# Kernel optimization log

Measured on AMD Instinct MI355X. Metric: run time of the kernel, lower is better.

Reference implementation:

```python
import jax, jax.numpy as jnp
import numpy as np

B, S, V = 16, 256, 32000
E, H, L, FFN, NC = 256, 8, 2, 1024, 4
DK = E // H
NQ = E  # n_qubits == hidden_dim == embed_dim (required by the module's shape constraints)
EPS = 1e-5


def qproj(x, theta):
    # Analytic simulation of: RX(x_k) encode + trainable RX(theta_k) + CNOT ladder + MeasureAll(PauliZ).
    # RX gates on the same wire compose; CNOT ladder maps Z_j -> Z_0...Z_j in Heisenberg picture, so
    # <Z_j> = prod_{k<=j} cos(x_k + theta_k)  (product state expectation).
    return jnp.cumprod(jnp.cos(x + theta), axis=-1)


def layernorm(x, g, b):
    m = x.mean(-1, keepdims=True)
    v = x.var(-1, keepdims=True)
    return (x - m) * jax.lax.rsqrt(v + EPS) * g + b


def sinusoidal_pe(seq, d):
    pos = jnp.arange(seq, dtype=jnp.float32)[:, None]
    div = jnp.exp(jnp.arange(0, d, 2, dtype=jnp.float32) * (-np.log(10000.0) / d))
    pe = jnp.zeros((seq, d), jnp.float32)
    pe = pe.at[:, 0::2].set(jnp.sin(pos * div)).at[:, 1::2].set(jnp.cos(pos * div))
    return pe


def _forward(x, token_emb, lstm_W, lstm_b, lstm_theta, ln1_g, ln1_b, ln2_g, ln2_b,
             qkv_theta, combine_W, combine_b, ffn_theta, lin1_W, lin1_b, lin2_W, lin2_b,
             cls_W, cls_b):
    emb = token_emb[x]  # (B, S, E)

    # --- QLSTM: each gate = linear -> quantum circuit -> nonlinearity ---
    def step(carry, xt):
        hx, cx = carry
        comb = jnp.concatenate([xt, hx], axis=-1)                      # (B, 2E)
        z = jnp.einsum('bd,gdq->gbq', comb, lstm_W) + lstm_b[:, None]  # (4, B, NQ)
        q = jnp.cumprod(jnp.cos(z + lstm_theta[:, None, :]), axis=-1)
        f = jax.nn.sigmoid(q[0])
        i = jax.nn.sigmoid(q[1])
        g = jnp.tanh(q[2])
        o = jax.nn.sigmoid(q[3])
        cx = f * cx + i * g
        hx = o * jnp.tanh(cx)
        return (hx, cx), hx

    h0 = jnp.zeros((emb.shape[0], NQ), emb.dtype)
    _, hs = jax.lax.scan(step, (h0, h0), jnp.swapaxes(emb, 0, 1))
    h = jnp.swapaxes(hs, 0, 1)  # (B, S, NQ)

    h = h + sinusoidal_pe(h.shape[1], E)[None]

    # --- quantum transformer blocks ---
    def heads(t):
        return t.reshape(t.shape[0], t.shape[1], H, DK).transpose(0, 2, 1, 3)

    for l in range(L):
        q = qproj(h, qkv_theta[l, 0])
        k = qproj(h, qkv_theta[l, 1])
        v = qproj(h, qkv_theta[l, 2])
        qh, kh, vh = heads(q), heads(k), heads(v)
        scores = jnp.einsum('bhqd,bhkd->bhqk', qh, kh) / jnp.sqrt(jnp.float32(DK))
        attn = jax.nn.softmax(scores, axis=-1)
        out = jnp.einsum('bhqk,bhkd->bhqd', attn, vh).transpose(0, 2, 1, 3).reshape(h.shape)
        out = out @ combine_W[l] + combine_b[l]
        h = layernorm(h + out, ln1_g[l], ln1_b[l])
        ff = qproj(h, ffn_theta[l]) @ lin1_W[l] + lin1_b[l]
        ff = jax.nn.relu(ff) @ lin2_W[l] + lin2_b[l]
        h = layernorm(h + ff, ln2_g[l], ln2_b[l])

    pooled = h.mean(axis=1)  # (B, E)
    return pooled @ cls_W + cls_b  # (B, NC)


def setup_inputs() -> dict:
    key = jax.random.key(0)
    ks = jax.random.split(key, 10)
    s = 0.05
    return {
        'x': jax.random.randint(ks[0], (B, S), 0, V),
        'token_emb': jax.random.normal(ks[1], (V, E), jnp.float32) * s,
        'lstm_W': jax.random.normal(ks[2], (4, 2 * E, NQ), jnp.float32) * s,
        'lstm_b': jnp.zeros((4, NQ), jnp.float32),
        'lstm_theta': jax.random.normal(ks[3], (4, NQ), jnp.float32) * s,
        'ln1_g': jnp.ones((L, E), jnp.float32),
        'ln1_b': jnp.zeros((L, E), jnp.float32),
        'ln2_g': jnp.ones((L, E), jnp.float32),
        'ln2_b': jnp.zeros((L, E), jnp.float32),
        'qkv_theta': jax.random.normal(ks[4], (L, 3, E), jnp.float32) * s,
        'combine_W': jax.random.normal(ks[5], (L, E, E), jnp.float32) * s,
        'combine_b': jnp.zeros((L, E), jnp.float32),
        'ffn_theta': jax.random.normal(ks[6], (L, E), jnp.float32) * s,
        'lin1_W': jax.random.normal(ks[7], (L, E, FFN), jnp.float32) * s,
        'lin1_b': jnp.zeros((L, FFN), jnp.float32),
        'lin2_W': jax.random.normal(ks[8], (L, FFN, E), jnp.float32) * s,
        'lin2_b': jnp.zeros((L, E), jnp.float32),
        'cls_W': jax.random.normal(ks[9], (E, NC), jnp.float32) * s,
        'cls_b': jnp.zeros((NC,), jnp.float32),
    }


def reference(x, token_emb, lstm_W, lstm_b, lstm_theta, ln1_g, ln1_b, ln2_g, ln2_b,
              qkv_theta, combine_W, combine_b, ffn_theta, lin1_W, lin1_b, lin2_W, lin2_b,
              cls_W, cls_b):
    return _forward(x, token_emb, lstm_W, lstm_b, lstm_theta, ln1_g, ln1_b, ln2_g, ln2_b,
                    qkv_theta, combine_W, combine_b, ffn_theta, lin1_W, lin1_b, lin2_W, lin2_b,
                    cls_W, cls_b)
```

## Files before the change

kernel.cpp:

```cpp
#include <hip/hip_runtime.h>
#include <hip/hip_bf16.h>


typedef __attribute__((ext_vector_type(8))) short bf8v;
typedef __attribute__((ext_vector_type(4))) float f4v;
#define MFMA16 __builtin_amdgcn_mfma_f32_16x16x32_bf16

__device__ __forceinline__ unsigned short f2bf(float f) {
  unsigned u = __builtin_bit_cast(unsigned, f);
  u += 0x7fffu + ((u >> 16) & 1u);
  return (unsigned short)(u >> 16);
}
__device__ __forceinline__ float rcp_f(float x) { return __builtin_amdgcn_rcpf(x); }
__device__ __forceinline__ float sigm(float x) { return rcp_f(1.f + __expf(-x)); }
__device__ __forceinline__ float tanh_f(float x) { return 1.f - 2.f * rcp_f(__expf(2.f * x) + 1.f); }

#define DOT2BF(acc, a, b) \
  asm("v_dot2_f32_bf16 %0, %1, %2, %0" : "+v"(acc) : "v"(a), "v"(b))

__global__ void embed_kernel(const int* __restrict__ x, const float* __restrict__ tab,
                             unsigned short* __restrict__ eb) {
  int tok = blockIdx.x, tid = threadIdx.x;
  eb[tok * 256 + tid] = f2bf(tab[x[tok] * 256 + tid]);
}

__global__ void pack_bt(const float* __restrict__ W, int K, int N,
                        unsigned short* __restrict__ Th, long wz, long tz) {
  __shared__ float tile[64][65];
  W += (long)blockIdx.z * wz;
  Th += (long)blockIdx.z * tz;
  int n0 = blockIdx.x * 64, k0 = blockIdx.y * 64;
  int tid = threadIdx.x, tx = tid & 63, ty = tid >> 6;
  for (int r = ty; r < 64; r += 4) tile[r][tx] = W[(k0 + r) * N + n0 + tx];
  __syncthreads();
  for (int r = ty; r < 64; r += 4) {
    Th[(n0 + r) * K + k0 + tx] = f2bf(tile[tx][r]);
  }
}

__global__ void pack_wreg_kernel(const float* __restrict__ lstmW, unsigned* __restrict__ Wreg) {
  int o = blockIdx.x * 256 + threadIdx.x;
  int c = o & 3;
  int q = (o >> 2) & 255;
  int i4 = (o >> 10) & 15;
  int gs = o >> 14;
  int gi = gs >> 1, s = gs & 1;
  int i = i4 * 4 + c;
  int d = s * 128 + 2 * i;
  unsigned lo = f2bf(lstmW[(gi * 512 + 256 + d) * 256 + q]);
  unsigned hi = f2bf(lstmW[(gi * 512 + 256 + d + 1) * 256 + q]);
  Wreg[o] = lo | (hi << 16);
}

__global__ void pack_wl_kernel(const float* __restrict__ lstmW, unsigned* __restrict__ WLg) {
  int o = blockIdx.x * 256 + threadIdx.x;
  int c = o & 3;
  int q = (o >> 2) & 255;
  int p4 = o >> 10;
  int d = 2 * (p4 * 4 + c);
  unsigned lo = f2bf(lstmW[(3 * 512 + 256 + d) * 256 + q]);
  unsigned hi = f2bf(lstmW[(3 * 512 + 256 + d + 1) * 256 + q]);
  WLg[o] = lo | (hi << 16);
}

__global__ void __launch_bounds__(256) gemm_mfma(const unsigned short* __restrict__ A,
                                                 const unsigned short* __restrict__ B,
                                                 const float* __restrict__ bias,
                                                 float* __restrict__ Cf,
                                                 unsigned short* __restrict__ Cb,
                                                 int M, int N, int K, int mode) {
  __shared__ unsigned short As[128 * 40];
  __shared__ unsigned short Bs[128 * 40];

  const int tid = threadIdx.x;
  const int lane = tid & 63;
  const int wid = tid >> 6;
  const int wr = wid >> 1, wc = wid & 1;
  const int bm = blockIdx.y * 128, bn = blockIdx.x * 128;

  const int srow = tid >> 2;
  const int scol = (tid & 3) * 8;

  f4v acc[4][4] = {};

  for (int kt = 0; kt < K; kt += 32) {
#pragma unroll
    for (int p = 0; p < 2; ++p) {
      int r = srow + p * 64;
      *(uint4*)(&As[r * 40 + scol]) = *(const uint4*)(&A[(bm + r) * K + kt + scol]);
      *(uint4*)(&Bs[r * 40 + scol]) = *(const uint4*)(&B[(bn + r) * K + kt + scol]);
    }
    __syncthreads();

    bf8v a[4], b[4];
    const int kq = (lane >> 4) * 8;
#pragma unroll
    for (int f = 0; f < 4; ++f) {
      a[f] = *(const bf8v*)(&As[(wr * 64 + f * 16 + (lane & 15)) * 40 + kq]);
      b[f] = *(const bf8v*)(&Bs[(wc * 64 + f * 16 + (lane & 15)) * 40 + kq]);
    }
#pragma unroll
    for (int fm = 0; fm < 4; ++fm)
#pragma unroll
      for (int fn = 0; fn < 4; ++fn)
        acc[fm][fn] = MFMA16(a[fm], b[fn], acc[fm][fn], 0, 0, 0);
    __syncthreads();
  }

#pragma unroll
  for (int fm = 0; fm < 4; ++fm)
#pragma unroll
    for (int fn = 0; fn < 4; ++fn) {
      int c = bn + wc * 64 + fn * 16 + (lane & 15);
      int r0 = bm + wr * 64 + fm * 16 + ((lane >> 4) << 2);
      float bv = bias[c];
#pragma unroll
      for (int j = 0; j < 4; ++j) {
        float v = acc[fm][fn][j] + bv;
        if (mode == 1) {
          Cb[(r0 + j) * N + c] = f2bf(fmaxf(v, 0.f));
        } else {
          Cf[(r0 + j) * N + c] = v;
        }
      }
    }
}

__global__ void
__attribute__((amdgpu_flat_work_group_size(512, 512), amdgpu_waves_per_eu(2, 2)))
lstm_kernel(const unsigned* __restrict__ Wreg,
            const unsigned* __restrict__ WLg,
            const float* __restrict__ lstmTh,
            const float* __restrict__ xw,
            float* __restrict__ hb) {
  extern __shared__ char smem[];
  unsigned* WL = (unsigned*)smem;
  float* part = (float*)(smem + 131072);
  float* qv = part + 2048;
  float* wtot = qv + 1024;
  unsigned* hp = (unsigned*)(wtot + 16);

  const int t = threadIdx.x;
  const int b = blockIdx.x;
  const int q = t & 255;
  const int s = t >> 8;
  const int lane = t & 63;
  const int w = t >> 6;

  {
    const uint4* src = (const uint4*)WLg;
    uint4* dst = (uint4*)WL;
    for (int j = t; j < 8192; j += 512) dst[j] = src[j];
  }
  const uint4* Wreg4 = (const uint4*)Wreg;
  uint4 wreg[48];
#pragma unroll
  for (int j = 0; j < 48; ++j) {
    int gi = j >> 4, i4 = j & 15;
    wreg[j] = Wreg4[((gi * 2 + s) * 16 + i4) * 256 + q];
  }
#pragma unroll
  for (int j = 0; j < 48; ++j) {
    asm volatile("" : "+v"(wreg[j].x), "+v"(wreg[j].y), "+v"(wreg[j].z), "+v"(wreg[j].w));
  }
  const float thA = lstmTh[t];
  const float thB = lstmTh[512 + t];
  float cx = 0.f;
  if (t < 128) hp[t] = 0u;
  __syncthreads();

  const int xbase = (b << 8) * 1024;
  const uint4* WL4 = (const uint4*)WL;
  const uint4* hp4 = (const uint4*)hp;

  float xa = xw[xbase + t];
  float xb = xw[xbase + 512 + t];

  for (int st = 0; st < 256; ++st) {
    int nx = (st < 255) ? st + 1 : 255;
    float xa_n = xw[xbase + nx * 1024 + t];
    float xb_n = xw[xbase + nx * 1024 + 512 + t];

    float a0 = 0.f, a1 = 0.f, a2 = 0.f, a3 = 0.f;
#pragma unroll
    for (int i4 = 0; i4 < 16; ++i4) {
      uint4 hh = hp4[(s << 4) + i4];
      uint4 w3 = WL4[((s << 4) + i4) * 256 + q];
      uint4 w0 = wreg[i4];
      uint4 w1 = wreg[16 + i4];
      uint4 w2 = wreg[32 + i4];
      DOT2BF(a0, w0.x, hh.x); DOT2BF(a0, w0.y, hh.y);
      DOT2BF(a0, w0.z, hh.z); DOT2BF(a0, w0.w, hh.w);
      DOT2BF(a1, w1.x, hh.x); DOT2BF(a1, w1.y, hh.y);
      DOT2BF(a1, w1.z, hh.z); DOT2BF(a1, w1.w, hh.w);
      DOT2BF(a2, w2.x, hh.x); DOT2BF(a2, w2.y, hh.y);
      DOT2BF(a2, w2.z, hh.z); DOT2BF(a2, w2.w, hh.w);
      DOT2BF(a3, w3.x, hh.x); DOT2BF(a3, w3.y, hh.y);
      DOT2BF(a3, w3.z, hh.z); DOT2BF(a3, w3.w, hh.w);
    }
    part[(0 * 2 + s) * 256 + q] = a0;
    part[(1 * 2 + s) * 256 + q] = a1;
    part[(2 * 2 + s) * 256 + q] = a2;
    part[(3 * 2 + s) * 256 + q] = a3;
    __syncthreads();

    int gA = s, gB = s + 2;
    float zA = part[(gA * 2 + 0) * 256 + q] + part[(gA * 2 + 1) * 256 + q] + xa + thA;
    float zB = part[(gB * 2 + 0) * 256 + q] + part[(gB * 2 + 1) * 256 + q] + xb + thB;
    float vA = __cosf(zA);
    float vB = __cosf(zB);
#pragma unroll
    for (int off = 1; off < 64; off <<= 1) {
      float oA = __shfl_up(vA, off, 64);
      float oB = __shfl_up(vB, off, 64);
      if (lane >= off) { vA *= oA; vB *= oB; }
    }
    if (lane == 63) { wtot[w * 2] = vA; wtot[w * 2 + 1] = vB; }
    qv[s * 256 + q] = vA;
    qv[512 + s * 256 + q] = vB;
    __syncthreads();

    if (t < 256) {
      int j = q >> 6;
      float p0 = 1.f, p1 = 1.f, p2 = 1.f, p3 = 1.f;
      for (int k = 0; k < j; ++k) {
        p0 *= wtot[2 * k];
        p1 *= wtot[2 * (4 + k)];
        p2 *= wtot[2 * k + 1];
        p3 *= wtot[2 * (4 + k) + 1];
      }
      float fg = sigm(qv[t] * p0);
      float ig = sigm(qv[256 + t] * p1);
      float gg = tanh_f(qv[512 + t] * p2);
      float og = sigm(qv[768 + t] * p3);
      cx = fg * cx + ig * gg;
      float hv = og * tanh_f(cx);
      hb[((b << 8) + st) * 256 + t] = hv;
      float nb = __shfl_xor(hv, 1, 64);
      if ((t & 1) == 0) hp[t >> 1] = (unsigned)f2bf(hv) | ((unsigned)f2bf(nb) << 16);
    }
    __syncthreads();
    xa = xa_n;
    xb = xb_n;
  }
}

__global__ void pe_add_kernel(float* __restrict__ h) {
  int tok = blockIdx.x, tid = threadIdx.x;
  int s = tok & 255;
  int j = tid >> 1;
  float div = __expf((float)j * -0.07195578415622253f);
  float ang = (float)s * div;
  float pe = (tid & 1) ? __cosf(ang) : __sinf(ang);
  h[tok * 256 + tid] += pe;
}

__global__ void qproj3_kernel(const float* __restrict__ hin, const float* __restrict__ thetas,
                              float* __restrict__ outbase) {
  __shared__ float wtot[4];
  int tok = blockIdx.x, y = blockIdx.y;
  int tid = threadIdx.x, lane = tid & 63, wid = tid >> 6;
  const float* theta = thetas + y * 256;
  float* out = outbase + (long)y * 1048576;
  float v = __cosf(hin[tok * 256 + tid] + theta[tid]);
#pragma unroll
  for (int off = 1; off < 64; off <<= 1) {
    float o = __shfl_up(v, off, 64);
    if (lane >= off) v *= o;
  }
  if (lane == 63) wtot[wid] = v;
  __syncthreads();
  float pre = 1.f;
  for (int w = 0; w < wid; ++w) pre *= wtot[w];
  out[tok * 256 + tid] = v * pre;
}

__global__ void qproj_bf_kernel(const float* __restrict__ hin, const float* __restrict__ theta,
                                unsigned short* __restrict__ outb) {
  __shared__ float wtot[4];
  int tok = blockIdx.x, tid = threadIdx.x, lane = tid & 63, wid = tid >> 6;
  float v = __cosf(hin[tok * 256 + tid] + theta[tid]);
#pragma unroll
  for (int off = 1; off < 64; off <<= 1) {
    float o = __shfl_up(v, off, 64);
    if (lane >= off) v *= o;
  }
  if (lane == 63) wtot[wid] = v;
  __syncthreads();
  float pre = 1.f;
  for (int w = 0; w < wid; ++w) pre *= wtot[w];
  outb[tok * 256 + tid] = f2bf(v * pre);
}

__global__ void __launch_bounds__(256, 1) attn_kernel(const float* __restrict__ qb,
                                                      const float* __restrict__ kb,
                                                      const float* __restrict__ vb,
                                                      unsigned short* __restrict__ outb) {
  extern __shared__ float sm[];
  float* Qs = sm;
  float* Ks = Qs + 256 * 36;
  float* Vs = Ks + 256 * 36;
  float* ps = Vs + 32 * 260;
  int hd = blockIdx.x, b = blockIdx.y;
  int tid = threadIdx.x, lane = tid & 63, wid = tid >> 6;
  const float scale = 0.17677669529663687f;

  for (int i = tid; i < 256 * 32; i += 256) {
    int r = i >> 5, d = i & 31;
    int src = (b * 256 + r) * 256 + hd * 32 + d;
    Qs[r * 36 + d] = qb[src];
    Ks[r * 36 + d] = kb[src];
    Vs[d * 260 + r] = vb[src];
  }
  __syncthreads();

  float* pw = ps + wid * 256;
  for (int r = wid; r < 256; r += 4) {
    float4 qreg[8];
    const float4* qrow = (const float4*)(Qs + r * 36);
#pragma unroll
    for (int i = 0; i < 8; ++i) qreg[i] = qrow[i];
    float s[4];
#pragma unroll
    for (int j = 0; j < 4; ++j) {
      int k = lane + 64 * j;
      const float4* kr = (const float4*)(Ks + k * 36);
      float a = 0.f;
#pragma unroll
      for (int i = 0; i < 8; ++i) {
        float4 kv = kr[i];
        a += qreg[i].x * kv.x + qreg[i].y * kv.y + qreg[i].z * kv.z + qreg[i].w * kv.w;
      }
      s[j] = a * scale;
    }
    float m = fmaxf(fmaxf(s[0], s[1]), fmaxf(s[2], s[3]));
#pragma unroll
    for (int off = 32; off; off >>= 1) m = fmaxf(m, __shfl_xor(m, off, 64));
    float p[4], sum = 0.f;
#pragma unroll
    for (int j = 0; j < 4; ++j) { p[j] = __expf(s[j] - m); sum += p[j]; }
#pragma unroll
    for (int off = 32; off; off >>= 1) sum += __shfl_xor(sum, off, 64);
    float inv = rcp_f(sum);
#pragma unroll
    for (int j = 0; j < 4; ++j) pw[lane + 64 * j] = p[j] * inv;
    int d = lane & 31, half = lane >> 5;
    const float4* pv = (const float4*)(pw + half * 128);
    const float4* v4 = (const float4*)(Vs + d * 260 + half * 128);
    float a = 0.f;
#pragma unroll
    for (int i = 0; i < 32; ++i) {
      float4 pp = pv[i];
      float4 vv = v4[i];
      a += pp.x * vv.x + pp.y * vv.y + pp.z * vv.z + pp.w * vv.w;
    }
    a += __shfl_down(a, 32, 64);
    if (lane < 32) outb[(b * 256 + r) * 256 + hd * 32 + d] = f2bf(a);
  }
}

__global__ void ln_kernel(float* __restrict__ hio, const float* __restrict__ delta,
                          const float* __restrict__ gamma, const float* __restrict__ beta) {
  __shared__ float red[16];
  int tok = blockIdx.x, tid = threadIdx.x, lane = tid & 63, wid = tid >> 6;
  float v = hio[tok * 256 + tid] + delta[tok * 256 + tid];
  float s1 = v, s2 = v * v;
#pragma unroll
  for (int off = 32; off; off >>= 1) {
    s1 += __shfl_xor(s1, off, 64);
    s2 += __shfl_xor(s2, off, 64);
  }
  if (lane == 0) { red[wid] = s1; red[wid + 8] = s2; }
  __syncthreads();
  float t1 = red[0] + red[1] + red[2] + red[3];
  float t2 = red[8] + red[9] + red[10] + red[11];
  float mean = t1 * (1.f / 256.f);
  float var = t2 * (1.f / 256.f) - mean * mean;
  float w = rsqrtf(var + 1e-5f);
  hio[tok * 256 + tid] = (v - mean) * w * gamma[tid] + beta[tid];
}

__global__ void pool_cls_kernel(const float* __restrict__ h, const float* __restrict__ clsW,
                                const float* __restrict__ clsb, float* __restrict__ out) {
  __shared__ float pl[256];
  __shared__ float red[8];
  int b = blockIdx.x, tid = threadIdx.x, lane = tid & 63, wid = tid >> 6;
  float s = 0.f;
  for (int t = 0; t < 256; ++t) s += h[(b * 256 + t) * 256 + tid];
  pl[tid] = s * (1.f / 256.f);
  __syncthreads();
  for (int c = 0; c < 4; ++c) {
    float v = pl[tid] * clsW[tid * 4 + c];
#pragma unroll
    for (int off = 32; off; off >>= 1) v += __shfl_xor(v, off, 64);
    if (lane == 0) red[wid] = v;
    __syncthreads();
    if (tid == 0) out[b * 4 + c] = red[0] + red[1] + red[2] + red[3] + clsb[c];
    __syncthreads();
  }
}

extern "C" void kernel_launch(void* const* d_in, const int* in_sizes, int n_in,
                              void* d_out, int out_size, void* d_ws, size_t ws_size,
                              hipStream_t stream) {
  const int* x = (const int*)d_in[0];
  const float* token_emb = (const float*)d_in[1];
  const float* lstm_W = (const float*)d_in[2];
  const float* lstm_b = (const float*)d_in[3];
  const float* lstm_th = (const float*)d_in[4];
  const float* ln1_g = (const float*)d_in[5];
  const float* ln1_b = (const float*)d_in[6];
  const float* ln2_g = (const float*)d_in[7];
  const float* ln2_b = (const float*)d_in[8];
  const float* qkv_th = (const float*)d_in[9];
  const float* comb_W = (const float*)d_in[10];
  const float* comb_b = (const float*)d_in[11];
  const float* ffn_th = (const float*)d_in[12];
  const float* lin1_W = (const float*)d_in[13];
  const float* lin1_b = (const float*)d_in[14];
  const float* lin2_W = (const float*)d_in[15];
  const float* lin2_b = (const float*)d_in[16];
  const float* cls_W = (const float*)d_in[17];
  const float* cls_b = (const float*)d_in[18];

  float* ws = (float*)d_ws;
  typedef unsigned short ushort_t;
  ushort_t* emb_b = (ushort_t*)ws;
  ushort_t* att_b = emb_b;
  float* xw = ws + 1048576;
  ushort_t* ffh_b = (ushort_t*)xw;
  float* hb = ws + 5242880;
  float* qq = ws + 6291456;
  float* kk = ws + 7340032;
  float* vv = ws + 8388608;
  float* tmp = ws + 9437184;
  unsigned* Wreg = (unsigned*)tmp;
  unsigned* WLg = (unsigned*)(tmp + 98304);
  ushort_t* ffq_b = (ushort_t*)(ws + 10485760);
  ushort_t* wxt_b = (ushort_t*)(ws + 11534336);
  ushort_t* cmb_b = wxt_b + 262144;
  ushort_t* l1_b = cmb_b + 131072;
  ushort_t* l2_b = l1_b + 524288;

  const int LSTM_LDS = 131072 + 8192 + 4096 + 64 + 512;
  const int ATT_LDS = (256 * 36 * 2 + 32 * 260 + 4 * 256) * 4;
  (void)hipFuncSetAttribute(reinterpret_cast<const void*>(lstm_kernel),
                            hipFuncAttributeMaxDynamicSharedMemorySize, LSTM_LDS);
  (void)hipFuncSetAttribute(reinterpret_cast<const void*>(attn_kernel),
                            hipFuncAttributeMaxDynamicSharedMemorySize, ATT_LDS);

  embed_kernel<<<4096, 256, 0, stream>>>(x, token_emb, emb_b);
  pack_wreg_kernel<<<384, 256, 0, stream>>>(lstm_W, Wreg);
  pack_wl_kernel<<<128, 256, 0, stream>>>(lstm_W, WLg);
  pack_bt<<<dim3(4, 4, 4), 256, 0, stream>>>(lstm_W, 256, 256, wxt_b, 131072, 65536);
  pack_bt<<<dim3(4, 4, 2), 256, 0, stream>>>(comb_W, 256, 256, cmb_b, 65536, 65536);
  pack_bt<<<dim3(16, 4, 2), 256, 0, stream>>>(lin1_W, 256, 1024, l1_b, 262144, 262144);
  pack_bt<<<dim3(4, 16, 2), 256, 0, stream>>>(lin2_W, 1024, 256, l2_b, 262144, 262144);

  gemm_mfma<<<dim3(8, 32), 256, 0, stream>>>(emb_b, wxt_b, lstm_b,
                                             xw, nullptr, 4096, 1024, 256, 0);
  lstm_kernel<<<16, 512, LSTM_LDS, stream>>>(Wreg, WLg, lstm_th, xw, hb);
  pe_add_kernel<<<4096, 256, 0, stream>>>(hb);

  for (int l = 0; l < 2; ++l) {
    qproj3_kernel<<<dim3(4096, 3), 256, 0, stream>>>(hb, qkv_th + l * 768, qq);
    attn_kernel<<<dim3(8, 16), 256, ATT_LDS, stream>>>(qq, kk, vv, att_b);
    gemm_mfma<<<dim3(2, 32), 256, 0, stream>>>(att_b, cmb_b + l * 65536, comb_b + l * 256,
                                               tmp, nullptr, 4096, 256, 256, 0);
    ln_kernel<<<4096, 256, 0, stream>>>(hb, tmp, ln1_g + l * 256, ln1_b + l * 256);
    qproj_bf_kernel<<<4096, 256, 0, stream>>>(hb, ffn_th + l * 256, ffq_b);
    gemm_mfma<<<dim3(8, 32), 256, 0, stream>>>(ffq_b, l1_b + l * 262144, lin1_b + l * 1024,
                                               nullptr, ffh_b, 4096, 1024, 256, 1);
    gemm_mfma<<<dim3(2, 32), 256, 0, stream>>>(ffh_b, l2_b + l * 262144, lin2_b + l * 256,
                                               tmp, nullptr, 4096, 256, 1024, 0);
    ln_kernel<<<4096, 256, 0, stream>>>(hb, tmp, ln2_g + l * 256, ln2_b + l * 256);
  }

  pool_cls_kernel<<<16, 256, 0, stream>>>(hb, cls_W, cls_b, (float*)d_out);
}
```

Before: 1.273 ms.

## Move LSTM weights to AGPRs, fuse PE/LN/qproj, add 64-tile GEMM, split pooling

```diff
diff --git a/kernel.cpp b/kernel.cpp
--- a/kernel.cpp
+++ b/kernel.cpp
@@ -125,6 +125,88 @@
       }
     }
 }
+
+__global__ void __launch_bounds__(256) gemm64(const unsigned short* __restrict__ A,
+                                              const unsigned short* __restrict__ B,
+                                              const float* __restrict__ bias,
+                                              float* __restrict__ Cf,
+                                              int M, int N, int K) {
+  __shared__ unsigned short As[64 * 40];
+  __shared__ unsigned short Bs[64 * 40];
+
+  const int tid = threadIdx.x;
+  const int lane = tid & 63;
+  const int wid = tid >> 6;
+  const int bm = blockIdx.y * 64, bn = blockIdx.x * 64;
+  const int srow = tid >> 2;
+  const int scol = (tid & 3) * 8;
+
+  f4v acc[4] = {};
+
+  for (int kt = 0; kt < K; kt += 32) {
+    *(uint4*)(&As[srow * 40 + scol]) = *(const uint4*)(&A[(bm + srow) * K + kt + scol]);
+    *(uint4*)(&Bs[srow * 40 + scol]) = *(const uint4*)(&B[(bn + srow) * K + kt + scol]);
+    __syncthreads();
+
+    const int kq = (lane >> 4) * 8;
+    bf8v a = *(const bf8v*)(&As[(wid * 16 + (lane & 15)) * 40 + kq]);
+#pragma unroll
+    for (int f = 0; f < 4; ++f) {
+      bf8v b = *(const bf8v*)(&Bs[(f * 16 + (lane & 15)) * 40 + kq]);
+      acc[f] = MFMA16(a, b, acc[f], 0, 0, 0);
+    }
+    __syncthreads();
+  }
+
+#pragma unroll
+  for (int f = 0; f < 4; ++f) {
+    int c = bn + f * 16 + (lane & 15);
+    int r0 = bm + wid * 16 + ((lane >> 4) << 2);
+    float bv = bias[c];
+#pragma unroll
+    for (int j = 0; j < 4; ++j) {
+      Cf[(r0 + j) * N + c] = acc[f][j] + bv;
+    }
+  }
+}
+
+#define DECLA4(gi, i4) \
+  unsigned ag##gi##_##i4##_0, ag##gi##_##i4##_1, ag##gi##_##i4##_2, ag##gi##_##i4##_3;
+#define DECLG(gi) \
+  DECLA4(gi, 0) DECLA4(gi, 1) DECLA4(gi, 2) DECLA4(gi, 3) \
+  DECLA4(gi, 4) DECLA4(gi, 5) DECLA4(gi, 6) DECLA4(gi, 7) \
+  DECLA4(gi, 8) DECLA4(gi, 9) DECLA4(gi, 10) DECLA4(gi, 11) \
+  DECLA4(gi, 12) DECLA4(gi, 13) DECLA4(gi, 14) DECLA4(gi, 15)
+
+#define LOADA4(gi, i4) { \
+  uint4 tw = Wreg4[(((gi) * 2 + s) * 16 + (i4)) * 256 + q]; \
+  asm volatile("v_accvgpr_write_b32 %0, %1" : "=a"(ag##gi##_##i4##_0) : "v"(tw.x)); \
+  asm volatile("v_accvgpr_write_b32 %0, %1" : "=a"(ag##gi##_##i4##_1) : "v"(tw.y)); \
+  asm volatile("v_accvgpr_write_b32 %0, %1" : "=a"(ag##gi##_##i4##_2) : "v"(tw.z)); \
+  asm volatile("v_accvgpr_write_b32 %0, %1" : "=a"(ag##gi##_##i4##_3) : "v"(tw.w)); }
+#define LOADG(gi) \
+  LOADA4(gi, 0) LOADA4(gi, 1) LOADA4(gi, 2) LOADA4(gi, 3) \
+  LOADA4(gi, 4) LOADA4(gi, 5) LOADA4(gi, 6) LOADA4(gi, 7) \
+  LOADA4(gi, 8) LOADA4(gi, 9) LOADA4(gi, 10) LOADA4(gi, 11) \
+  LOADA4(gi, 12) LOADA4(gi, 13) LOADA4(gi, 14) LOADA4(gi, 15)
+
+#define DOTA1(acc, areg, hw) { unsigned t_; \
+  asm("v_accvgpr_read_b32 %1, %2\n\tv_dot2_f32_bf16 %0, %1, %3, %0" \
+      : "+v"(acc), "=&v"(t_) : "a"(areg), "v"(hw)); }
+#define DOTA(acc, gi, i4, hh) \
+  DOTA1(acc, ag##gi##_##i4##_0, (hh).x) \
+  DOTA1(acc, ag##gi##_##i4##_1, (hh).y) \
+  DOTA1(acc, ag##gi##_##i4##_2, (hh).z) \
+  DOTA1(acc, ag##gi##_##i4##_3, (hh).w)
+
+#define CHUNKA(i4) { \
+  uint4 hh = hp4[(s << 4) + (i4)]; \
+  uint4 w3 = WL4[((s << 4) + (i4)) * 256 + q]; \
+  DOTA(a0, 0, i4, hh) \
+  DOTA(a1, 1, i4, hh) \
+  DOTA(a2, 2, i4, hh) \
+  DOT2BF(a3, w3.x, hh.x); DOT2BF(a3, w3.y, hh.y); \
+  DOT2BF(a3, w3.z, hh.z); DOT2BF(a3, w3.w, hh.w); }
 
 __global__ void
 __attribute__((amdgpu_flat_work_group_size(512, 512), amdgpu_waves_per_eu(2, 2)))
@@ -153,16 +235,8 @@
     for (int j = t; j < 8192; j += 512) dst[j] = src[j];
   }
   const uint4* Wreg4 = (const uint4*)Wreg;
-  uint4 wreg[48];
-#pragma unroll
-  for (int j = 0; j < 48; ++j) {
-    int gi = j >> 4, i4 = j & 15;
-    wreg[j] = Wreg4[((gi * 2 + s) * 16 + i4) * 256 + q];
-  }
-#pragma unroll
-  for (int j = 0; j < 48; ++j) {
-    asm volatile("" : "+v"(wreg[j].x), "+v"(wreg[j].y), "+v"(wreg[j].z), "+v"(wreg[j].w));
-  }
+  DECLG(0) DECLG(1) DECLG(2)
+  LOADG(0) LOADG(1) LOADG(2)
   const float thA = lstmTh[t];
   const float thB = lstmTh[512 + t];
   float cx = 0.f;
@@ -175,6 +249,7 @@
 
   float xa = xw[xbase + t];
   float xb = xw[xbase + 512 + t];
+  const float pediv = __expf((float)(q >> 1) * -0.07195578415622253f);
 
   for (int st = 0; st < 256; ++st) {
     int nx = (st < 255) ? st + 1 : 255;
@@ -182,22 +257,10 @@
     float xb_n = xw[xbase + nx * 1024 + 512 + t];
 
     float a0 = 0.f, a1 = 0.f, a2 = 0.f, a3 = 0.f;
-#pragma unroll
-    for (int i4 = 0; i4 < 16; ++i4) {
-      uint4 hh = hp4[(s << 4) + i4];
-      uint4 w3 = WL4[((s << 4) + i4) * 256 + q];
-      uint4 w0 = wreg[i4];
-      uint4 w1 = wreg[16 + i4];
-      uint4 w2 = wreg[32 + i4];
-      DOT2BF(a0, w0.x, hh.x); DOT2BF(a0, w0.y, hh.y);
-      DOT2BF(a0, w0.z, hh.z); DOT2BF(a0, w0.w, hh.w);
-      DOT2BF(a1, w1.x, hh.x); DOT2BF(a1, w1.y, hh.y);
-      DOT2BF(a1, w1.z, hh.z); DOT2BF(a1, w1.w, hh.w);
-      DOT2BF(a2, w2.x, hh.x); DOT2BF(a2, w2.y, hh.y);
-      DOT2BF(a2, w2.z, hh.z); DOT2BF(a2, w2.w, hh.w);
-      DOT2BF(a3, w3.x, hh.x); DOT2BF(a3, w3.y, hh.y);
-      DOT2BF(a3, w3.z, hh.z); DOT2BF(a3, w3.w, hh.w);
-    }
+    CHUNKA(0) CHUNKA(1) CHUNKA(2) CHUNKA(3)
+    CHUNKA(4) CHUNKA(5) CHUNKA(6) CHUNKA(7)
+    CHUNKA(8) CHUNKA(9) CHUNKA(10) CHUNKA(11)
+    CHUNKA(12) CHUNKA(13) CHUNKA(14) CHUNKA(15)
     part[(0 * 2 + s) * 256 + q] = a0;
     part[(1 * 2 + s) * 256 + q] = a1;
     part[(2 * 2 + s) * 256 + q] = a2;
@@ -235,7 +298,9 @@
       float og = sigm(qv[768 + t] * p3);
       cx = fg * cx + ig * gg;
       float hv = og * tanh_f(cx);
-      hb[((b << 8) + st) * 256 + t] = hv;
+      float ang = (float)st * pediv;
+      float pe = (q & 1) ? __cosf(ang) : __sinf(ang);
+      hb[((b << 8) + st) * 256 + q] = hv + pe;
       float nb = __shfl_xor(hv, 1, 64);
       if ((t & 1) == 0) hp[t >> 1] = (unsigned)f2bf(hv) | ((unsigned)f2bf(nb) << 16);
     }
@@ -243,16 +308,6 @@
     xa = xa_n;
     xb = xb_n;
   }
-}
-
-__global__ void pe_add_kernel(float* __restrict__ h) {
-  int tok = blockIdx.x, tid = threadIdx.x;
-  int s = tok & 255;
-  int j = tid >> 1;
-  float div = __expf((float)j * -0.07195578415622253f);
-  float ang = (float)s * div;
-  float pe = (tid & 1) ? __cosf(ang) : __sinf(ang);
-  h[tok * 256 + tid] += pe;
 }
 
 __global__ void qproj3_kernel(const float* __restrict__ hin, const float* __restrict__ thetas,
@@ -275,21 +330,40 @@
   out[tok * 256 + tid] = v * pre;
 }
 
-__global__ void qproj_bf_kernel(const float* __restrict__ hin, const float* __restrict__ theta,
+__global__ void ln_qproj_kernel(float* __restrict__ hio, const float* __restrict__ delta,
+                                const float* __restrict__ gamma, const float* __restrict__ beta,
+                                const float* __restrict__ theta,
                                 unsigned short* __restrict__ outb) {
+  __shared__ float red[16];
   __shared__ float wtot[4];
   int tok = blockIdx.x, tid = threadIdx.x, lane = tid & 63, wid = tid >> 6;
-  float v = __cosf(hin[tok * 256 + tid] + theta[tid]);
+  float v = hio[tok * 256 + tid] + delta[tok * 256 + tid];
+  float s1 = v, s2 = v * v;
+#pragma unroll
+  for (int off = 32; off; off >>= 1) {
+    s1 += __shfl_xor(s1, off, 64);
+    s2 += __shfl_xor(s2, off, 64);
+  }
+  if (lane == 0) { red[wid] = s1; red[wid + 8] = s2; }
+  __syncthreads();
+  float t1 = red[0] + red[1] + red[2] + red[3];
+  float t2 = red[8] + red[9] + red[10] + red[11];
+  float mean = t1 * (1.f / 256.f);
+  float var = t2 * (1.f / 256.f) - mean * mean;
+  float w = rsqrtf(var + 1e-5f);
+  float val = (v - mean) * w * gamma[tid] + beta[tid];
+  hio[tok * 256 + tid] = val;
+  float c = __cosf(val + theta[tid]);
 #pragma unroll
   for (int off = 1; off < 64; off <<= 1) {
-    float o = __shfl_up(v, off, 64);
-    if (lane >= off) v *= o;
-  }
-  if (lane == 63) wtot[wid] = v;
+    float o = __shfl_up(c, off, 64);
+    if (lane >= off) c *= o;
+  }
+  if (lane == 63) wtot[wid] = c;
   __syncthreads();
   float pre = 1.f;
-  for (int w = 0; w < wid; ++w) pre *= wtot[w];
-  outb[tok * 256 + tid] = f2bf(v * pre);
+  for (int k = 0; k < wid; ++k) pre *= wtot[k];
+  outb[tok * 256 + tid] = f2bf(c * pre);
 }
 
 __global__ void __launch_bounds__(256, 1) attn_kernel(const float* __restrict__ qb,
@@ -380,13 +454,22 @@
   hio[tok * 256 + tid] = (v - mean) * w * gamma[tid] + beta[tid];
 }
 
-__global__ void pool_cls_kernel(const float* __restrict__ h, const float* __restrict__ clsW,
-                                const float* __restrict__ clsb, float* __restrict__ out) {
+__global__ void poolA_kernel(const float* __restrict__ h, float* __restrict__ partial) {
+  int bx = blockIdx.x;
+  int b = bx >> 4, ch = bx & 15;
+  int tid = threadIdx.x;
+  float s = 0.f;
+  for (int tt = ch * 16; tt < ch * 16 + 16; ++tt) s += h[((b << 8) + tt) * 256 + tid];
+  partial[bx * 256 + tid] = s;
+}
+
+__global__ void poolB_kernel(const float* __restrict__ partial, const float* __restrict__ clsW,
+                             const float* __restrict__ clsb, float* __restrict__ out) {
   __shared__ float pl[256];
   __shared__ float red[8];
   int b = blockIdx.x, tid = threadIdx.x, lane = tid & 63, wid = tid >> 6;
   float s = 0.f;
-  for (int t = 0; t < 256; ++t) s += h[(b * 256 + t) * 256 + tid];
+  for (int ch = 0; ch < 16; ++ch) s += partial[(b * 16 + ch) * 256 + tid];
   pl[tid] = s * (1.f / 256.f);
   __syncthreads();
   for (int c = 0; c < 4; ++c) {
@@ -441,6 +524,7 @@
   ushort_t* cmb_b = wxt_b + 262144;
   ushort_t* l1_b = cmb_b + 131072;
   ushort_t* l2_b = l1_b + 524288;
+  float* partial = ws + 12255232;
 
   const int LSTM_LDS = 131072 + 8192 + 4096 + 64 + 512;
   const int ATT_LDS = (256 * 36 * 2 + 32 * 260 + 4 * 256) * 4;
@@ -460,21 +544,21 @@
   gemm_mfma<<<dim3(8, 32), 256, 0, stream>>>(emb_b, wxt_b, lstm_b,
                                              xw, nullptr, 4096, 1024, 256, 0);
   lstm_kernel<<<16, 512, LSTM_LDS, stream>>>(Wreg, WLg, lstm_th, xw, hb);
-  pe_add_kernel<<<4096, 256, 0, stream>>>(hb);
 
   for (int l = 0; l < 2; ++l) {
     qproj3_kernel<<<dim3(4096, 3), 256, 0, stream>>>(hb, qkv_th + l * 768, qq);
     attn_kernel<<<dim3(8, 16), 256, ATT_LDS, stream>>>(qq, kk, vv, att_b);
-    gemm_mfma<<<dim3(2, 32), 256, 0, stream>>>(att_b, cmb_b + l * 65536, comb_b + l * 256,
-                                               tmp, nullptr, 4096, 256, 256, 0);
-    ln_kernel<<<4096, 256, 0, stream>>>(hb, tmp, ln1_g + l * 256, ln1_b + l * 256);
-    qproj_bf_kernel<<<4096, 256, 0, stream>>>(hb, ffn_th + l * 256, ffq_b);
+    gemm64<<<dim3(4, 64), 256, 0, stream>>>(att_b, cmb_b + l * 65536, comb_b + l * 256,
+                                            tmp, 4096, 256, 256);
+    ln_qproj_kernel<<<4096, 256, 0, stream>>>(hb, tmp, ln1_g + l * 256, ln1_b + l * 256,
+                                              ffn_th + l * 256, ffq_b);
     gemm_mfma<<<dim3(8, 32), 256, 0, stream>>>(ffq_b, l1_b + l * 262144, lin1_b + l * 1024,
                                                nullptr, ffh_b, 4096, 1024, 256, 1);
-    gemm_mfma<<<dim3(2, 32), 256, 0, stream>>>(ffh_b, l2_b + l * 262144, lin2_b + l * 256,
-                                               tmp, nullptr, 4096, 256, 1024, 0);
+    gemm64<<<dim3(4, 64), 256, 0, stream>>>(ffh_b, l2_b + l * 262144, lin2_b + l * 256,
+                                            tmp, 4096, 256, 1024);
     ln_kernel<<<4096, 256, 0, stream>>>(hb, tmp, ln2_g + l * 256, ln2_b + l * 256);
   }
 
-  pool_cls_kernel<<<16, 256, 0, stream>>>(hb, cls_W, cls_b, (float*)d_out);
-}
+  poolA_kernel<<<256, 256, 0, stream>>>(hb, partial);
+  poolB_kernel<<<16, 256, 0, stream>>>(partial, cls_W, cls_b, (float*)d_out);
+}
```

Result: slower. 1.529 ms (+20.1%).
